# Performance work log

Measured on AMD Instinct MI355X. Metric: run time of the kernel, lower is better.

## Reference

```python
import jax, jax.numpy as jnp
import numpy as np

LEVEL = 3  # matches init_kwargs
# pywt Wavelet('db4').rec_lo (synthesis low-pass, 8 taps)
REC_LO = np.array([
    0.23037781330885523, 0.7148465705525415, 0.6308807679295904,
    -0.02798376941698385, -0.18703481171888114, 0.030841381835986965,
    0.032883011666982945, -0.010597401784997278], dtype=np.float32)


def _rec_filters():
    rec_lo = jnp.asarray(REC_LO)
    L = rec_lo.shape[0]
    # QMF relation: rec_hi[k] = (-1)^k * rec_lo[L-1-k]
    signs = jnp.asarray((-1.0) ** np.arange(L), dtype=rec_lo.dtype)
    rec_hi = rec_lo[::-1] * signs
    return rec_lo, rec_hi


def _iswt(coeffs, rec_lo, rec_hi):
    """Inverse stationary (undecimated / a-trous) wavelet transform.

    coeffs = [cA_L, cD_L, cD_{L-1}, ..., cD_1], each of shape [BN, T].
    Perfect reconstruction for the circular-padded dilated-conv SWT
    (ptwt/pywt convention): at each level with dilation d,
      x[n] = 0.5 * sum_m rec_lo[m]*a[(n - d*(m - L//2 + 1)) % T]
                 + rec_hi[m]*cd[(n - d*(m - L//2 + 1)) % T]
    """
    L = rec_lo.shape[0]
    n_lev = len(coeffs) - 1
    res = coeffs[0]
    for c_pos in range(n_lev):
        hi = coeffs[1 + c_pos]
        d = 2 ** (n_lev - 1 - c_pos)
        acc = jnp.zeros_like(res)
        for m in range(L):  # static 8-tap loop, unrolled under jit
            shift = d * (m - L // 2 + 1)
            acc = acc + rec_lo[m] * jnp.roll(res, shift, axis=-1) \
                      + rec_hi[m] * jnp.roll(hi, shift, axis=-1)
        res = 0.5 * acc
    return res


def setup_inputs() -> dict:
    key = jax.random.key(0)
    B, N, T = 32, 64, 4096
    x = jax.random.normal(key, (B, (LEVEL + 1) * N, T), dtype=jnp.float32)
    return {"x": x}


def reference(x):
    B, expanded_N, T = x.shape
    N = expanded_N // (LEVEL + 1)
    xr = x.reshape(B * N, LEVEL + 1, T)  # (B,N,level+1,T) merged over B,N
    coeffs = [xr[:, i, :] for i in range(LEVEL + 1)]
    rec_lo, rec_hi = _rec_filters()
    rec = _iswt(coeffs, rec_lo, rec_hi)  # [B*N, T]
    return rec.reshape(B, N, T)
```

## Files before the change

### kernel.cpp

```cpp
#include <hip/hip_runtime.h>


namespace {

constexpr int TT = 4096;
constexpr int T4 = TT / 4;
constexpr int NT = 256;

template <int D, bool LAST>
__device__ __forceinline__ void iswt_level(const float4* __restrict__ gsrc,
                                           float* lds_res, float* lds_hi,
                                           float4* __restrict__ dst4, int t) {
  constexpr float LO[8] = {
      0.23037781330885523f,  0.7148465705525415f,  0.6308807679295904f,
      -0.02798376941698385f, -0.18703481171888114f, 0.030841381835986965f,
      0.032883011666982945f, -0.010597401784997278f};
  constexpr float HI[8] = {
      -0.010597401784997278f, -0.032883011666982945f, 0.030841381835986965f,
      0.18703481171888114f,   -0.02798376941698385f,  -0.6308807679295904f,
      0.7148465705525415f,    -0.23037781330885523f};

  float4* hiw4 = reinterpret_cast<float4*>(lds_hi);
#pragma unroll
  for (int k = 0; k < 4; ++k) hiw4[t + k * NT] = gsrc[t + k * NT];
  __syncthreads();

  constexpr int W4 = (7 * D + 7) / 4;
  const float4* res4 = reinterpret_cast<const float4*>(lds_res);
  const float4* hir4 = reinterpret_cast<const float4*>(lds_hi);

  float4 acc[4];
#pragma unroll
  for (int g = 0; g < 4; ++g) {
    const int c = t + g * NT;
    float w[4 * W4];

#pragma unroll
    for (int i = 0; i < W4; ++i) {
      const float4 v = res4[(c - D + i) & (T4 - 1)];
      w[4 * i + 0] = v.x; w[4 * i + 1] = v.y;
      w[4 * i + 2] = v.z; w[4 * i + 3] = v.w;
    }
    float a0 = 0.f, a1 = 0.f, a2 = 0.f, a3 = 0.f;
#pragma unroll
    for (int m = 0; m < 8; ++m) {
      const int o = D * (7 - m);
      a0 += LO[m] * w[o + 0];
      a1 += LO[m] * w[o + 1];
      a2 += LO[m] * w[o + 2];
      a3 += LO[m] * w[o + 3];
    }

#pragma unroll
    for (int i = 0; i < W4; ++i) {
      const float4 v = hir4[(c - D + i) & (T4 - 1)];
      w[4 * i + 0] = v.x; w[4 * i + 1] = v.y;
      w[4 * i + 2] = v.z; w[4 * i + 3] = v.w;
    }
#pragma unroll
    for (int m = 0; m < 8; ++m) {
      const int o = D * (7 - m);
      a0 += HI[m] * w[o + 0];
      a1 += HI[m] * w[o + 1];
      a2 += HI[m] * w[o + 2];
      a3 += HI[m] * w[o + 3];
    }
    acc[g] = make_float4(0.5f * a0, 0.5f * a1, 0.5f * a2, 0.5f * a3);
  }

  __syncthreads();
#pragma unroll
  for (int g = 0; g < 4; ++g) dst4[t + g * NT] = acc[g];
  if (!LAST) __syncthreads();
}

__global__ __launch_bounds__(NT) void iswt_kernel(const float* __restrict__ x,
                                                  float* __restrict__ out) {
  __shared__ __align__(16) float lds_res[TT];
  __shared__ __align__(16) float lds_hi[TT];

  const int t = threadIdx.x;
  const int row = blockIdx.x;

  const float4* xr4 = reinterpret_cast<const float4*>(x) + (size_t)row * 4 * T4;
  float4* res4 = reinterpret_cast<float4*>(lds_res);

#pragma unroll
  for (int k = 0; k < 4; ++k) res4[t + k * NT] = xr4[t + k * NT];

  iswt_level<4, false>(xr4 + 1 * T4, lds_res, lds_hi, res4, t);
  iswt_level<2, false>(xr4 + 2 * T4, lds_res, lds_hi, res4, t);
  float4* out4 = reinterpret_cast<float4*>(out) + (size_t)row * T4;
  iswt_level<1, true>(xr4 + 3 * T4, lds_res, lds_hi, out4, t);
}

}

extern "C" void kernel_launch(void* const* d_in, const int* in_sizes, int n_in,
                              void* d_out, int out_size, void* d_ws, size_t ws_size,
                              hipStream_t stream) {
  const float* x = reinterpret_cast<const float*>(d_in[0]);
  float* out = reinterpret_cast<float*>(d_out);
  const int rows = out_size / TT;
  iswt_kernel<<<rows, NT, 0, stream>>>(x, out);
}
```

Before: 202.4 us.

## Prefetch all coefficient rows into registers up front and merge level barriers

All four global coefficient rows are loaded into registers at kernel start, so every global read is in flight together instead of being serialized behind each level's compute and barriers. The hi-band LDS write is merged with the result write-back, which removes one barrier per level, and launch bounds request four blocks per CU. This costs 64 extra VGPRs of prefetched data per thread, which may reduce occupancy or force spills.

```diff
diff --git a/kernel.cpp b/kernel.cpp
--- a/kernel.cpp
+++ b/kernel.cpp
@@ -7,10 +7,10 @@
 constexpr int T4 = TT / 4;
 constexpr int NT = 256;
 
-template <int D, bool LAST>
-__device__ __forceinline__ void iswt_level(const float4* __restrict__ gsrc,
-                                           float* lds_res, float* lds_hi,
-                                           float4* __restrict__ dst4, int t) {
+template <int D>
+__device__ __forceinline__ void level_compute(const float* lds_res,
+                                              const float* lds_hi,
+                                              int t, float4 acc[4]) {
   constexpr float LO[8] = {
       0.23037781330885523f,  0.7148465705525415f,  0.6308807679295904f,
       -0.02798376941698385f, -0.18703481171888114f, 0.030841381835986965f,
@@ -20,16 +20,10 @@
       0.18703481171888114f,   -0.02798376941698385f,  -0.6308807679295904f,
       0.7148465705525415f,    -0.23037781330885523f};
 
-  float4* hiw4 = reinterpret_cast<float4*>(lds_hi);
-#pragma unroll
-  for (int k = 0; k < 4; ++k) hiw4[t + k * NT] = gsrc[t + k * NT];
-  __syncthreads();
-
   constexpr int W4 = (7 * D + 7) / 4;
   const float4* res4 = reinterpret_cast<const float4*>(lds_res);
   const float4* hir4 = reinterpret_cast<const float4*>(lds_hi);
 
-  float4 acc[4];
 #pragma unroll
   for (int g = 0; g < 4; ++g) {
     const int c = t + g * NT;
@@ -67,15 +61,10 @@
     }
     acc[g] = make_float4(0.5f * a0, 0.5f * a1, 0.5f * a2, 0.5f * a3);
   }
-
-  __syncthreads();
-#pragma unroll
-  for (int g = 0; g < 4; ++g) dst4[t + g * NT] = acc[g];
-  if (!LAST) __syncthreads();
 }
 
-__global__ __launch_bounds__(NT) void iswt_kernel(const float* __restrict__ x,
-                                                  float* __restrict__ out) {
+__global__ __launch_bounds__(NT, 4) void iswt_kernel(const float* __restrict__ x,
+                                                     float* __restrict__ out) {
   __shared__ __align__(16) float lds_res[TT];
   __shared__ __align__(16) float lds_hi[TT];
 
@@ -83,15 +72,50 @@
   const int row = blockIdx.x;
 
   const float4* xr4 = reinterpret_cast<const float4*>(x) + (size_t)row * 4 * T4;
+
+  float4 rA[4], rH3[4], rH2[4], rH1[4];
+#pragma unroll
+  for (int k = 0; k < 4; ++k) rA[k]  = xr4[0 * T4 + t + k * NT];
+#pragma unroll
+  for (int k = 0; k < 4; ++k) rH3[k] = xr4[1 * T4 + t + k * NT];
+#pragma unroll
+  for (int k = 0; k < 4; ++k) rH2[k] = xr4[2 * T4 + t + k * NT];
+#pragma unroll
+  for (int k = 0; k < 4; ++k) rH1[k] = xr4[3 * T4 + t + k * NT];
+
   float4* res4 = reinterpret_cast<float4*>(lds_res);
+  float4* hiw4 = reinterpret_cast<float4*>(lds_hi);
 
 #pragma unroll
-  for (int k = 0; k < 4; ++k) res4[t + k * NT] = xr4[t + k * NT];
+  for (int k = 0; k < 4; ++k) res4[t + k * NT] = rA[k];
+#pragma unroll
+  for (int k = 0; k < 4; ++k) hiw4[t + k * NT] = rH3[k];
+  __syncthreads();
 
-  iswt_level<4, false>(xr4 + 1 * T4, lds_res, lds_hi, res4, t);
-  iswt_level<2, false>(xr4 + 2 * T4, lds_res, lds_hi, res4, t);
+  float4 acc[4];
+
+  level_compute<4>(lds_res, lds_hi, t, acc);
+  __syncthreads();
+#pragma unroll
+  for (int k = 0; k < 4; ++k) {
+    res4[t + k * NT] = acc[k];
+    hiw4[t + k * NT] = rH2[k];
+  }
+  __syncthreads();
+
+  level_compute<2>(lds_res, lds_hi, t, acc);
+  __syncthreads();
+#pragma unroll
+  for (int k = 0; k < 4; ++k) {
+    res4[t + k * NT] = acc[k];
+    hiw4[t + k * NT] = rH1[k];
+  }
+  __syncthreads();
+
+  level_compute<1>(lds_res, lds_hi, t, acc);
   float4* out4 = reinterpret_cast<float4*>(out) + (size_t)row * T4;
-  iswt_level<1, true>(xr4 + 3 * T4, lds_res, lds_hi, out4, t);
+#pragma unroll
+  for (int k = 0; k < 4; ++k) out4[t + k * NT] = acc[k];
 }
 
 }
```

Result: slower. 214.3 us (+5.9%).

## Prefetch all coefficient rows into LDS with async global_load_lds double buffering

Applied to the files above, without the earlier changes.

Replaces the per-level synchronous global-to-register-to-LDS copies with direct global_load_lds DMA. The first three coefficient rows are issued up front, and the fourth row's load is issued while levels one and two compute. Detail bands use two LDS buffers, and manual s_waitcnt/s_barrier counts sequence the stages. The aim is to hide global memory latency behind compute and drop register staging, at the cost of 50% more LDS per block, which may lower occupancy. Correctness depends on hand-tuned vmcnt counts.

```diff
diff --git a/kernel.cpp b/kernel.cpp
--- a/kernel.cpp
+++ b/kernel.cpp
@@ -7,10 +7,15 @@
 constexpr int T4 = TT / 4;
 constexpr int NT = 256;
 
-template <int D, bool LAST>
-__device__ __forceinline__ void iswt_level(const float4* __restrict__ gsrc,
-                                           float* lds_res, float* lds_hi,
-                                           float4* __restrict__ dst4, int t) {
+#define GLD16(gp, lp)                                                      \
+  __builtin_amdgcn_global_load_lds(                                        \
+      (const __attribute__((address_space(1))) void*)(gp),                 \
+      (__attribute__((address_space(3))) void*)(lp), 16, 0, 0)
+
+template <int D>
+__device__ __forceinline__ void level_compute(const float* lds_res,
+                                              const float* lds_hi,
+                                              int t, float4 acc[4]) {
   constexpr float LO[8] = {
       0.23037781330885523f,  0.7148465705525415f,  0.6308807679295904f,
       -0.02798376941698385f, -0.18703481171888114f, 0.030841381835986965f,
@@ -20,16 +25,10 @@
       0.18703481171888114f,   -0.02798376941698385f,  -0.6308807679295904f,
       0.7148465705525415f,    -0.23037781330885523f};
 
-  float4* hiw4 = reinterpret_cast<float4*>(lds_hi);
-#pragma unroll
-  for (int k = 0; k < 4; ++k) hiw4[t + k * NT] = gsrc[t + k * NT];
-  __syncthreads();
-
   constexpr int W4 = (7 * D + 7) / 4;
   const float4* res4 = reinterpret_cast<const float4*>(lds_res);
   const float4* hir4 = reinterpret_cast<const float4*>(lds_hi);
 
-  float4 acc[4];
 #pragma unroll
   for (int g = 0; g < 4; ++g) {
     const int c = t + g * NT;
@@ -67,31 +66,57 @@
     }
     acc[g] = make_float4(0.5f * a0, 0.5f * a1, 0.5f * a2, 0.5f * a3);
   }
-
-  __syncthreads();
-#pragma unroll
-  for (int g = 0; g < 4; ++g) dst4[t + g * NT] = acc[g];
-  if (!LAST) __syncthreads();
 }
 
 __global__ __launch_bounds__(NT) void iswt_kernel(const float* __restrict__ x,
                                                   float* __restrict__ out) {
   __shared__ __align__(16) float lds_res[TT];
-  __shared__ __align__(16) float lds_hi[TT];
+  __shared__ __align__(16) float lds_hiA[TT];
+  __shared__ __align__(16) float lds_hiB[TT];
 
   const int t = threadIdx.x;
   const int row = blockIdx.x;
 
-  const float4* xr4 = reinterpret_cast<const float4*>(x) + (size_t)row * 4 * T4;
+  const float* xr = x + (size_t)row * 4 * TT;
+
+#pragma unroll
+  for (int k = 0; k < 4; ++k)
+    GLD16(xr + 0 * TT + (t + k * NT) * 4, lds_res + (t + k * NT) * 4);
+#pragma unroll
+  for (int k = 0; k < 4; ++k)
+    GLD16(xr + 1 * TT + (t + k * NT) * 4, lds_hiA + (t + k * NT) * 4);
+#pragma unroll
+  for (int k = 0; k < 4; ++k)
+    GLD16(xr + 2 * TT + (t + k * NT) * 4, lds_hiB + (t + k * NT) * 4);
+
+  asm volatile("s_waitcnt vmcnt(4)\n\ts_barrier" ::: "memory");
+
+  float4 acc[4];
   float4* res4 = reinterpret_cast<float4*>(lds_res);
 
+  level_compute<4>(lds_res, lds_hiA, t, acc);
+  asm volatile("s_waitcnt lgkmcnt(0)\n\ts_barrier" ::: "memory");
+
 #pragma unroll
-  for (int k = 0; k < 4; ++k) res4[t + k * NT] = xr4[t + k * NT];
+  for (int k = 0; k < 4; ++k)
+    GLD16(xr + 3 * TT + (t + k * NT) * 4, lds_hiA + (t + k * NT) * 4);
+#pragma unroll
+  for (int k = 0; k < 4; ++k) res4[t + k * NT] = acc[k];
 
-  iswt_level<4, false>(xr4 + 1 * T4, lds_res, lds_hi, res4, t);
-  iswt_level<2, false>(xr4 + 2 * T4, lds_res, lds_hi, res4, t);
+  asm volatile("s_waitcnt vmcnt(4) lgkmcnt(0)\n\ts_barrier" ::: "memory");
+
+  level_compute<2>(lds_res, lds_hiB, t, acc);
+  asm volatile("s_waitcnt lgkmcnt(0)\n\ts_barrier" ::: "memory");
+
+#pragma unroll
+  for (int k = 0; k < 4; ++k) res4[t + k * NT] = acc[k];
+
+  asm volatile("s_waitcnt vmcnt(0) lgkmcnt(0)\n\ts_barrier" ::: "memory");
+
+  level_compute<1>(lds_res, lds_hiA, t, acc);
   float4* out4 = reinterpret_cast<float4*>(out) + (size_t)row * T4;
-  iswt_level<1, true>(xr4 + 3 * T4, lds_res, lds_hi, out4, t);
+#pragma unroll
+  for (int k = 0; k < 4; ++k) out4[t + k * NT] = acc[k];
 }
 
 }
```

Measured after the change: 201.2 us. About the same (-0.6%).
